# Kernel optimization log

Measured on AMD Instinct MI355X. Metric: run time of the kernel, lower is better.

The kernel has to match this reference:

```python
import jax, jax.numpy as jnp
import numpy as np

N_NODES = 50000
N_EDGES = 800000
D_IN = 128
D_OUT = 128
D_RED = 32  # out_features // reduction
ORDER = 3


def setup_inputs() -> dict:
    key = jax.random.key(0)
    ks = jax.random.split(key, 16)
    s = 1.0 / np.sqrt(D_IN)
    inp = {
        'features': jax.random.normal(ks[0], (N_NODES, D_IN), jnp.float32),
        'edge_row': jax.random.randint(ks[1], (N_EDGES,), 0, N_NODES, jnp.int32),
        'edge_col': jax.random.randint(ks[2], (N_EDGES,), 0, N_NODES, jnp.int32),
        'edge_val': jax.random.uniform(ks[3], (N_EDGES,), jnp.float32) / 16.0,  # ~1/avg_degree normalization
        'w1': jax.random.normal(ks[4], (D_IN, D_OUT), jnp.float32) * s,
        'b1': jax.random.normal(ks[5], (D_OUT,), jnp.float32) * s,
        'w2': jax.random.normal(ks[6], (D_IN, D_OUT), jnp.float32) * s,
        'b2': jax.random.normal(ks[7], (D_OUT,), jnp.float32) * s,
        'w3': jax.random.normal(ks[8], (D_IN, D_OUT), jnp.float32) * s,
        'b3': jax.random.normal(ks[9], (D_OUT,), jnp.float32) * s,
        'fc1_w': jax.random.normal(ks[10], (D_OUT, D_RED), jnp.float32) * s,
        'fc1_b': jax.random.normal(ks[11], (D_RED,), jnp.float32) * s,
        'fc2_w': jax.random.normal(ks[12], (D_RED, D_OUT), jnp.float32) * (1.0 / np.sqrt(D_RED)),
        'fc2_b': jax.random.normal(ks[13], (D_OUT,), jnp.float32) * s,
    }
    return inp


def reference(features, edge_row, edge_col, edge_val, w1, b1, w2, b2, w3, b3,
              fc1_w, fc1_b, fc2_w, fc2_b):
    def spmm(x):  # sparse [N,N] @ dense [N,D] via gather + segment_sum
        msgs = edge_val[:, None] * x[edge_col]          # [E, D]
        return jax.ops.segment_sum(msgs, edge_row, num_segments=N_NODES)

    def ngnn(w, b, order):
        h = jnp.tanh(features @ w)                      # active=True path
        for _ in range(order):                          # order spmm hops
            h = spmm(h)
        return h + b

    abstract = [ngnn(w, b, k + 1) for k, (w, b) in enumerate([(w1, b1), (w2, b2), (w3, b3)])]
    feats = jnp.stack(abstract, axis=0)                 # [order, N, D]
    m = jnp.mean(feats, axis=1)                         # [order, D]
    a = jax.nn.relu(m @ fc1_w + fc1_b) @ fc2_w + fc2_b  # [order, D]
    a = jax.nn.softmax(a, axis=0)                       # softmax over order dim
    out = jnp.einsum('ond,od->nd', feats, a)            # weighted combine
    return out
```

## Files before the change

### kernel.cpp

```cpp
#include <hip/hip_runtime.h>
#include <cstdint>

#define N_NODES 50000
#define N_EDGES 800000
#define EPCAP 64

typedef _Float16 half8 __attribute__((ext_vector_type(8)));
typedef float f32x4 __attribute__((ext_vector_type(4)));


__device__ inline unsigned pack_half2(float lo, float hi) {
    union { _Float16 h[2]; unsigned u; } cv;
    cv.h[0] = (_Float16)lo; cv.h[1] = (_Float16)hi;
    return cv.u;
}
__device__ inline float h_lo(unsigned u) {
    union { unsigned u; _Float16 h[2]; } cv; cv.u = u; return (float)cv.h[0];
}
__device__ inline float h_hi(unsigned u) {
    union { unsigned u; _Float16 h[2]; } cv; cv.u = u; return (float)cv.h[1];
}


__global__ __launch_bounds__(256) void scatter_wprep_kernel(const int* __restrict__ rows,
                                                            const int* __restrict__ cols,
                                                            const float* __restrict__ vals,
                                                            int* __restrict__ cnt,
                                                            unsigned* __restrict__ ep,
                                                            const float* __restrict__ w3,
                                                            const float* __restrict__ w2,
                                                            const float* __restrict__ w1,
                                                            _Float16* __restrict__ Wt) {
    int bx = blockIdx.x;
    if (bx >= 3125) {
        int b = bx - 3125;
        const float* W = (b == 0) ? w3 : (b == 1) ? w2 : w1;
        _Float16* O = Wt + (size_t)b * 16384;
        for (int i = threadIdx.x; i < 16384; i += 256) {
            int j = i >> 7, d = i & 127;
            O[j * 128 + d] = (_Float16)W[d * 128 + j];
        }
        return;
    }
    int e = bx * 256 + threadIdx.x;
    int r = rows[e];
    int p = atomicAdd(&cnt[r], 1);
    union { _Float16 h; unsigned short s; } cv; cv.h = (_Float16)vals[e];
    if (p < EPCAP)
        __builtin_nontemporal_store(((unsigned)cv.s << 16) | (unsigned)cols[e],
                                    &ep[(size_t)r * EPCAP + p]);
}


__global__ __launch_bounds__(256) void gemm_mfma3_kernel(const float* __restrict__ F,
                                                         const _Float16* __restrict__ Wt,
                                                         unsigned* __restrict__ T1, int nrows) {
    __shared__ _Float16 Fs[64 * 128];
    __shared__ _Float16 Ws[128 * 128];
    int tid = threadIdx.x;
    int lane = tid & 63, wv = tid >> 6;
    int c = lane & 15, g = lane >> 4;
    int rowbase = blockIdx.x * 64;

    for (int i = tid; i < 4096; i += 256) {
        int r = i >> 6;
        int row = rowbase + r; if (row >= nrows) row = nrows - 1;
        float2 fv = ((const float2*)F)[(size_t)row * 64 + (i & 63)];
        *(unsigned*)((char*)Fs + ((i * 4) ^ ((r & 15) << 4))) = pack_half2(fv.x, fv.y);
    }
    __syncthreads();

    half8 afr[4];
    #pragma unroll
    for (int ks = 0; ks < 4; ++ks) {
        int off = (((wv * 16 + c) * 128 + ks * 32 + g * 8) * 2) ^ (c << 4);
        afr[ks] = *(const half8*)((const char*)Fs + off);
    }

    for (int b = 0; b < 3; ++b) {
        const unsigned* WtU = (const unsigned*)(Wt + (size_t)b * 16384);
        for (int i = tid; i < 8192; i += 256) {
            int j = i >> 6;
            *(unsigned*)((char*)Ws + ((i * 4) ^ ((j & 15) << 4))) = WtU[i];
        }
        __syncthreads();

        f32x4 zero = {0.f, 0.f, 0.f, 0.f};
        f32x4 acc[8];
        #pragma unroll
        for (int t = 0; t < 8; ++t) acc[t] = zero;

        #pragma unroll
        for (int ks = 0; ks < 4; ++ks) {
            #pragma unroll
            for (int t = 0; t < 8; ++t) {
                int j = t * 16 + c;
                int off = ((j * 128 + ks * 32 + g * 8) * 2) ^ ((j & 15) << 4);
                half8 bfr = *(const half8*)((const char*)Ws + off);
                acc[t] = __builtin_amdgcn_mfma_f32_16x16x32_f16(afr[ks], bfr, acc[t], 0, 0, 0);
            }
        }

        #pragma unroll
        for (int t = 0; t < 4; ++t) {
            int j = t * 16 + c;
            #pragma unroll
            for (int r = 0; r < 4; ++r) {
                int row = rowbase + wv * 16 + g * 4 + r;
                if (row < N_NODES)
                    T1[(size_t)row * 192 + b * 64 + j] =
                        pack_half2(tanhf(acc[t][r]), tanhf(acc[t + 4][r]));
            }
        }
        __syncthreads();
    }
}


template <int NCHUNK>
__global__ __launch_bounds__(512) void spmm_stage_kernel(const int* __restrict__ cnts,
                                                         const unsigned* __restrict__ ep,
                                                         const unsigned* __restrict__ x,
                                                         unsigned* __restrict__ ob0,
                                                         unsigned* __restrict__ obf,
                                                         float* __restrict__ csumK) {
    __shared__ float cs[128];
    int tid = threadIdx.x;
    if (tid < 128) cs[tid] = 0.f;
    __syncthreads();

    int row = blockIdx.x * 8 + (tid >> 6);
    int lane = tid & 63;
    int n = __builtin_amdgcn_readfirstlane(cnts[row]);
    n = n < EPCAP ? n : EPCAP;
    const unsigned* e0 = ep + (size_t)row * EPCAP;

    float ax[NCHUNK], ay[NCHUNK];
    #pragma unroll
    for (int cc = 0; cc < NCHUNK; ++cc) { ax[cc] = 0.f; ay[cc] = 0.f; }

    const unsigned* xl = x + lane;
    constexpr int U = 8;
    int i = 0;
    for (; i + U <= n; i += U) {
        unsigned p[U];
        #pragma unroll
        for (int u = 0; u < U; ++u) p[u] = e0[i + u];
        unsigned gx[U][NCHUNK];
        #pragma unroll
        for (int u = 0; u < U; ++u) {
            unsigned b = (p[u] & 0xFFFFu) * (unsigned)(NCHUNK * 64);
            #pragma unroll
            for (int cc = 0; cc < NCHUNK; ++cc) gx[u][cc] = xl[b + cc * 64];
        }
        #pragma unroll
        for (int u = 0; u < U; ++u) {
            union { unsigned short s; _Float16 h; } cu; cu.s = (unsigned short)(p[u] >> 16);
            float v = (float)cu.h;
            #pragma unroll
            for (int cc = 0; cc < NCHUNK; ++cc) {
                ax[cc] += v * h_lo(gx[u][cc]);
                ay[cc] += v * h_hi(gx[u][cc]);
            }
        }
    }
    for (; i < n; ++i) {
        unsigned p = e0[i];
        unsigned b = (p & 0xFFFFu) * (unsigned)(NCHUNK * 64);
        union { unsigned short s; _Float16 h; } cu; cu.s = (unsigned short)(p >> 16);
        float v = (float)cu.h;
        #pragma unroll
        for (int cc = 0; cc < NCHUNK; ++cc) {
            unsigned gg = xl[b + cc * 64];
            ax[cc] += v * h_lo(gg);
            ay[cc] += v * h_hi(gg);
        }
    }

    #pragma unroll
    for (int cc = 0; cc < NCHUNK - 1; ++cc)
        ob0[(size_t)row * ((NCHUNK - 1) * 64) + cc * 64 + lane] = pack_half2(ax[cc], ay[cc]);

    float fx = ax[NCHUNK - 1], fy = ay[NCHUNK - 1];
    obf[(size_t)row * 64 + lane] = pack_half2(fx, fy);
    atomicAdd(&cs[2 * lane + 0], fx);
    atomicAdd(&cs[2 * lane + 1], fy);
    __syncthreads();
    if (tid < 128) atomicAdd(&csumK[(blockIdx.x & 7) * 384 + tid], cs[tid]);
}


__global__ __launch_bounds__(256) void combine_kernel(float* __restrict__ out,
                                                      const unsigned* __restrict__ f1,
                                                      const unsigned* __restrict__ f2,
                                                      const unsigned* __restrict__ f3,
                                                      const float* __restrict__ csum,
                                                      const float* __restrict__ b1,
                                                      const float* __restrict__ b2,
                                                      const float* __restrict__ b3,
                                                      const float* __restrict__ fc1w,
                                                      const float* __restrict__ fc1b,
                                                      const float* __restrict__ fc2w,
                                                      const float* __restrict__ fc2b) {
    __shared__ float m[3][128];
    __shared__ float rr[3][32];
    __shared__ float wgt[3][128];
    int t = threadIdx.x;

    if (t < 128) {
        const float inv = 1.0f / (float)N_NODES;
        int slot = (t < 64) ? (2 * t) : (2 * (t - 64) + 1);
        #pragma unroll
        for (int k = 0; k < 3; ++k) {
            float s = 0.f;
            #pragma unroll
            for (int rep = 0; rep < 8; ++rep) s += csum[rep * 384 + k * 128 + slot];
            const float* bk = (k == 0) ? b1 : (k == 1) ? b2 : b3;
            m[k][t] = s * inv + bk[t];
        }
    }
    __syncthreads();
    if (t < 96) {
        int k = t >> 5, j = t & 31;
        float acc = fc1b[j];
        for (int d = 0; d < 128; ++d) acc += m[k][d] * fc1w[d * 32 + j];
        rr[k][j] = fmaxf(acc, 0.f);
    }
    __syncthreads();
    if (t < 128) {
        float a[3];
        #pragma unroll
        for (int k = 0; k < 3; ++k) {
            float acc = fc2b[t];
            for (int j = 0; j < 32; ++j) acc += rr[k][j] * fc2w[j * 128 + t];
            a[k] = acc;
        }
        float mx = fmaxf(a[0], fmaxf(a[1], a[2]));
        float e0 = expf(a[0] - mx), e1 = expf(a[1] - mx), e2 = expf(a[2] - mx);
        float s = e0 + e1 + e2;
        wgt[0][t] = e0 / s;
        wgt[1][t] = e1 / s;
        wgt[2][t] = e2 / s;
    }
    __syncthreads();

    const int total = N_NODES * 32;
    int idx0 = blockIdx.x * blockDim.x + threadIdx.x;
    int stride = gridDim.x * blockDim.x;
    int qb = idx0 & 31;
    float4 W0 = *(const float4*)&wgt[0][qb * 4];
    float4 W1 = *(const float4*)&wgt[1][qb * 4];
    float4 W2 = *(const float4*)&wgt[2][qb * 4];
    float4 B1 = ((const float4*)b1)[qb];
    float4 B2 = ((const float4*)b2)[qb];
    float4 B3 = ((const float4*)b3)[qb];
    bool hi = qb >= 16;
    int qm = qb & 15;
    for (int idx = idx0; idx < total; idx += stride) {
        int row = idx >> 5;
        uint4 u1 = ((const uint4*)f1)[row * 16 + qm];
        uint4 u2 = ((const uint4*)f2)[row * 16 + qm];
        uint4 u3 = ((const uint4*)f3)[row * 16 + qm];
        float f1x = hi ? h_hi(u1.x) : h_lo(u1.x);
        float f1y = hi ? h_hi(u1.y) : h_lo(u1.y);
        float f1z = hi ? h_hi(u1.z) : h_lo(u1.z);
        float f1w = hi ? h_hi(u1.w) : h_lo(u1.w);
        float f2x = hi ? h_hi(u2.x) : h_lo(u2.x);
        float f2y = hi ? h_hi(u2.y) : h_lo(u2.y);
        float f2z = hi ? h_hi(u2.z) : h_lo(u2.z);
        float f2w = hi ? h_hi(u2.w) : h_lo(u2.w);
        float f3x = hi ? h_hi(u3.x) : h_lo(u3.x);
        float f3y = hi ? h_hi(u3.y) : h_lo(u3.y);
        float f3z = hi ? h_hi(u3.z) : h_lo(u3.z);
        float f3w = hi ? h_hi(u3.w) : h_lo(u3.w);
        float4 o;
        o.x = (f1x + B1.x) * W0.x + (f2x + B2.x) * W1.x + (f3x + B3.x) * W2.x;
        o.y = (f1y + B1.y) * W0.y + (f2y + B2.y) * W1.y + (f3y + B3.y) * W2.y;
        o.z = (f1z + B1.z) * W0.z + (f2z + B2.z) * W1.z + (f3z + B3.z) * W2.z;
        o.w = (f1w + B1.w) * W0.w + (f2w + B2.w) * W1.w + (f3w + B3.w) * W2.w;
        ((float4*)out)[idx] = o;
    }
}


extern "C" void kernel_launch(void* const* d_in, const int* in_sizes, int n_in,
                              void* d_out, int out_size, void* d_ws, size_t ws_size,
                              hipStream_t stream) {
    const float* F    = (const float*)d_in[0];
    const int*   erow = (const int*)d_in[1];
    const int*   ecol = (const int*)d_in[2];
    const float* eval_ = (const float*)d_in[3];
    const float* w1 = (const float*)d_in[4];  const float* b1 = (const float*)d_in[5];
    const float* w2 = (const float*)d_in[6];  const float* b2 = (const float*)d_in[7];
    const float* w3 = (const float*)d_in[8];  const float* b3 = (const float*)d_in[9];
    const float* fc1w = (const float*)d_in[10]; const float* fc1b = (const float*)d_in[11];
    const float* fc2w = (const float*)d_in[12]; const float* fc2b = (const float*)d_in[13];
    float* out = (float*)d_out;

    char* ws = (char*)d_ws;
    size_t off = 0;
    auto alloc = [&](size_t bytes) -> void* {
        off = (off + 255) & ~(size_t)255;
        void* p = ws + off;
        off += bytes;
        return p;
    };
    unsigned* T1   = (unsigned*)alloc((size_t)N_NODES * 192 * 4);
    unsigned* T2   = (unsigned*)alloc((size_t)N_NODES * 128 * 4);
    unsigned* T3   = (unsigned*)alloc((size_t)N_NODES * 64 * 4);
    unsigned* f1h  = (unsigned*)alloc((size_t)N_NODES * 64 * 4);
    unsigned* ep   = (unsigned*)alloc((size_t)N_NODES * EPCAP * 4);
    int*   counts  = (int*)alloc((size_t)N_NODES * sizeof(int));
    float* csum    = (float*)alloc(8 * 3 * 128 * sizeof(float));
    _Float16* Wt   = (_Float16*)alloc(3 * 16384 * sizeof(_Float16));
    unsigned* f2h  = T1;
    unsigned* f3h  = T1 + (size_t)N_NODES * 64;

    size_t zlen = (size_t)((char*)csum + 8 * 3 * 128 * sizeof(float) - (char*)counts);
    hipMemsetAsync(counts, 0, zlen, stream);

    scatter_wprep_kernel<<<3125 + 3, 256, 0, stream>>>(erow, ecol, eval_, counts, ep,
                                                       w3, w2, w1, Wt);
    gemm_mfma3_kernel<<<(N_NODES + 63) / 64, 256, 0, stream>>>(F, Wt, T1, N_NODES);

    const int spmmGrid = N_NODES / 8;

    spmm_stage_kernel<3><<<spmmGrid, 512, 0, stream>>>(counts, ep, T1, T2, f1h, csum + 0 * 128);
    spmm_stage_kernel<2><<<spmmGrid, 512, 0, stream>>>(counts, ep, T2, T3, f2h, csum + 1 * 128);
    spmm_stage_kernel<1><<<spmmGrid, 512, 0, stream>>>(counts, ep, T3, nullptr, f3h, csum + 2 * 128);

    combine_kernel<<<2048, 256, 0, stream>>>(out, f1h, f2h, f3h, csum, b1, b2, b3,
                                             fc1w, fc1b, fc2w, fc2b);
}
```

Measured before the change: 352.1 us.

## Fuse final SpMM hop with combine using column-sum trick for third-order mean

```diff
diff --git a/kernel.cpp b/kernel.cpp
--- a/kernel.cpp
+++ b/kernel.cpp
@@ -27,6 +27,7 @@
                                                             const float* __restrict__ vals,
                                                             int* __restrict__ cnt,
                                                             unsigned* __restrict__ ep,
+                                                            float* __restrict__ qsum,
                                                             const float* __restrict__ w3,
                                                             const float* __restrict__ w2,
                                                             const float* __restrict__ w1,
@@ -44,11 +45,13 @@
     }
     int e = bx * 256 + threadIdx.x;
     int r = rows[e];
+    int c = cols[e];
     int p = atomicAdd(&cnt[r], 1);
     union { _Float16 h; unsigned short s; } cv; cv.h = (_Float16)vals[e];
     if (p < EPCAP)
-        __builtin_nontemporal_store(((unsigned)cv.s << 16) | (unsigned)cols[e],
+        __builtin_nontemporal_store(((unsigned)cv.s << 16) | (unsigned)c,
                                     &ep[(size_t)r * EPCAP + p]);
+    atomicAdd(&qsum[c], (float)cv.h);
 }
 
 
@@ -117,13 +120,12 @@
 }
 
 
-template <int NCHUNK>
-__global__ __launch_bounds__(512) void spmm_stage_kernel(const int* __restrict__ cnts,
-                                                         const unsigned* __restrict__ ep,
-                                                         const unsigned* __restrict__ x,
-                                                         unsigned* __restrict__ ob0,
-                                                         unsigned* __restrict__ obf,
-                                                         float* __restrict__ csumK) {
+__global__ __launch_bounds__(512) void spmm1_kernel(const int* __restrict__ cnts,
+                                                    const unsigned* __restrict__ ep,
+                                                    const unsigned* __restrict__ x,
+                                                    unsigned* __restrict__ ob0,
+                                                    unsigned* __restrict__ obf,
+                                                    float* __restrict__ csum) {
     __shared__ float cs[128];
     int tid = threadIdx.x;
     if (tid < 128) cs[tid] = 0.f;
@@ -135,10 +137,7 @@
     n = n < EPCAP ? n : EPCAP;
     const unsigned* e0 = ep + (size_t)row * EPCAP;
 
-    float ax[NCHUNK], ay[NCHUNK];
-    #pragma unroll
-    for (int cc = 0; cc < NCHUNK; ++cc) { ax[cc] = 0.f; ay[cc] = 0.f; }
-
+    float ax[3] = {0.f, 0.f, 0.f}, ay[3] = {0.f, 0.f, 0.f};
     const unsigned* xl = x + lane;
     constexpr int U = 8;
     int i = 0;
@@ -146,19 +145,19 @@
         unsigned p[U];
         #pragma unroll
         for (int u = 0; u < U; ++u) p[u] = e0[i + u];
-        unsigned gx[U][NCHUNK];
+        unsigned gx[U][3];
         #pragma unroll
         for (int u = 0; u < U; ++u) {
-            unsigned b = (p[u] & 0xFFFFu) * (unsigned)(NCHUNK * 64);
+            unsigned b = (p[u] & 0xFFFFu) * 192u;
             #pragma unroll
-            for (int cc = 0; cc < NCHUNK; ++cc) gx[u][cc] = xl[b + cc * 64];
+            for (int cc = 0; cc < 3; ++cc) gx[u][cc] = xl[b + cc * 64];
         }
         #pragma unroll
         for (int u = 0; u < U; ++u) {
             union { unsigned short s; _Float16 h; } cu; cu.s = (unsigned short)(p[u] >> 16);
             float v = (float)cu.h;
             #pragma unroll
-            for (int cc = 0; cc < NCHUNK; ++cc) {
+            for (int cc = 0; cc < 3; ++cc) {
                 ax[cc] += v * h_lo(gx[u][cc]);
                 ay[cc] += v * h_hi(gx[u][cc]);
             }
@@ -166,120 +165,194 @@
     }
     for (; i < n; ++i) {
         unsigned p = e0[i];
-        unsigned b = (p & 0xFFFFu) * (unsigned)(NCHUNK * 64);
+        unsigned b = (p & 0xFFFFu) * 192u;
         union { unsigned short s; _Float16 h; } cu; cu.s = (unsigned short)(p >> 16);
         float v = (float)cu.h;
         #pragma unroll
-        for (int cc = 0; cc < NCHUNK; ++cc) {
+        for (int cc = 0; cc < 3; ++cc) {
             unsigned gg = xl[b + cc * 64];
             ax[cc] += v * h_lo(gg);
             ay[cc] += v * h_hi(gg);
         }
     }
 
-    #pragma unroll
-    for (int cc = 0; cc < NCHUNK - 1; ++cc)
-        ob0[(size_t)row * ((NCHUNK - 1) * 64) + cc * 64 + lane] = pack_half2(ax[cc], ay[cc]);
-
-    float fx = ax[NCHUNK - 1], fy = ay[NCHUNK - 1];
-    obf[(size_t)row * 64 + lane] = pack_half2(fx, fy);
-    atomicAdd(&cs[2 * lane + 0], fx);
-    atomicAdd(&cs[2 * lane + 1], fy);
-    __syncthreads();
-    if (tid < 128) atomicAdd(&csumK[(blockIdx.x & 7) * 384 + tid], cs[tid]);
-}
-
-
-__global__ __launch_bounds__(256) void combine_kernel(float* __restrict__ out,
-                                                      const unsigned* __restrict__ f1,
-                                                      const unsigned* __restrict__ f2,
-                                                      const unsigned* __restrict__ f3,
-                                                      const float* __restrict__ csum,
-                                                      const float* __restrict__ b1,
-                                                      const float* __restrict__ b2,
-                                                      const float* __restrict__ b3,
-                                                      const float* __restrict__ fc1w,
-                                                      const float* __restrict__ fc1b,
-                                                      const float* __restrict__ fc2w,
-                                                      const float* __restrict__ fc2b) {
+    ob0[(size_t)row * 128 + 0 * 64 + lane] = pack_half2(ax[0], ay[0]);
+    ob0[(size_t)row * 128 + 1 * 64 + lane] = pack_half2(ax[1], ay[1]);
+    obf[(size_t)row * 64 + lane] = pack_half2(ax[2], ay[2]);
+    atomicAdd(&cs[2 * lane + 0], ax[2]);
+    atomicAdd(&cs[2 * lane + 1], ay[2]);
+    __syncthreads();
+    if (tid < 128) atomicAdd(&csum[(blockIdx.x & 7) * 384 + tid], cs[tid]);
+}
+
+
+__global__ __launch_bounds__(512) void spmm2_kernel(const int* __restrict__ cnts,
+                                                    const unsigned* __restrict__ ep,
+                                                    const unsigned* __restrict__ x,
+                                                    unsigned* __restrict__ T3,
+                                                    unsigned* __restrict__ f2h,
+                                                    const float* __restrict__ qsum,
+                                                    float* __restrict__ csum) {
+    __shared__ float cs[256];
+    int tid = threadIdx.x;
+    if (tid < 256) cs[tid] = 0.f;
+    __syncthreads();
+
+    int row = blockIdx.x * 8 + (tid >> 6);
+    int lane = tid & 63;
+    int n = __builtin_amdgcn_readfirstlane(cnts[row]);
+    n = n < EPCAP ? n : EPCAP;
+    const unsigned* e0 = ep + (size_t)row * EPCAP;
+
+    float ax0 = 0.f, ay0 = 0.f, ax1 = 0.f, ay1 = 0.f;
+    const unsigned* xl = x + lane;
+    constexpr int U = 8;
+    int i = 0;
+    for (; i + U <= n; i += U) {
+        unsigned p[U];
+        #pragma unroll
+        for (int u = 0; u < U; ++u) p[u] = e0[i + u];
+        unsigned g0[U], g1[U];
+        #pragma unroll
+        for (int u = 0; u < U; ++u) {
+            unsigned b = (p[u] & 0xFFFFu) * 128u;
+            g0[u] = xl[b];
+            g1[u] = xl[b + 64];
+        }
+        #pragma unroll
+        for (int u = 0; u < U; ++u) {
+            union { unsigned short s; _Float16 h; } cu; cu.s = (unsigned short)(p[u] >> 16);
+            float v = (float)cu.h;
+            ax0 += v * h_lo(g0[u]); ay0 += v * h_hi(g0[u]);
+            ax1 += v * h_lo(g1[u]); ay1 += v * h_hi(g1[u]);
+        }
+    }
+    for (; i < n; ++i) {
+        unsigned p = e0[i];
+        unsigned b = (p & 0xFFFFu) * 128u;
+        union { unsigned short s; _Float16 h; } cu; cu.s = (unsigned short)(p >> 16);
+        float v = (float)cu.h;
+        unsigned g0 = xl[b], g1 = xl[b + 64];
+        ax0 += v * h_lo(g0); ay0 += v * h_hi(g0);
+        ax1 += v * h_lo(g1); ay1 += v * h_hi(g1);
+    }
+
+    T3[(size_t)row * 64 + lane] = pack_half2(ax0, ay0);
+    float qr = qsum[row];
+    atomicAdd(&cs[128 + 2 * lane + 0], qr * ax0);
+    atomicAdd(&cs[128 + 2 * lane + 1], qr * ay0);
+    f2h[(size_t)row * 64 + lane] = pack_half2(ax1, ay1);
+    atomicAdd(&cs[2 * lane + 0], ax1);
+    atomicAdd(&cs[2 * lane + 1], ay1);
+    __syncthreads();
+    if (tid < 256) atomicAdd(&csum[(blockIdx.x & 7) * 384 + 128 + tid], cs[tid]);
+}
+
+
+__global__ __launch_bounds__(512) void spmm3_combine_kernel(const int* __restrict__ cnts,
+                                                            const unsigned* __restrict__ ep,
+                                                            const unsigned* __restrict__ x,
+                                                            const unsigned* __restrict__ f1h,
+                                                            const unsigned* __restrict__ f2h,
+                                                            const float* __restrict__ csum,
+                                                            const float* __restrict__ b1,
+                                                            const float* __restrict__ b2,
+                                                            const float* __restrict__ b3,
+                                                            const float* __restrict__ fc1w,
+                                                            const float* __restrict__ fc1b,
+                                                            const float* __restrict__ fc2w,
+                                                            const float* __restrict__ fc2b,
+                                                            float* __restrict__ out) {
     __shared__ float m[3][128];
     __shared__ float rr[3][32];
-    __shared__ float wgt[3][128];
-    int t = threadIdx.x;
-
-    if (t < 128) {
+    __shared__ float wgtS[3][128];
+    int tid = threadIdx.x;
+
+    if (tid < 128) {
         const float inv = 1.0f / (float)N_NODES;
-        int slot = (t < 64) ? (2 * t) : (2 * (t - 64) + 1);
+        int slot = (tid < 64) ? (2 * tid) : (2 * (tid - 64) + 1);
         #pragma unroll
         for (int k = 0; k < 3; ++k) {
             float s = 0.f;
             #pragma unroll
             for (int rep = 0; rep < 8; ++rep) s += csum[rep * 384 + k * 128 + slot];
             const float* bk = (k == 0) ? b1 : (k == 1) ? b2 : b3;
-            m[k][t] = s * inv + bk[t];
-        }
-    }
-    __syncthreads();
-    if (t < 96) {
-        int k = t >> 5, j = t & 31;
+            m[k][tid] = s * inv + bk[tid];
+        }
+    }
+    __syncthreads();
+    if (tid < 96) {
+        int k = tid >> 5, j = tid & 31;
         float acc = fc1b[j];
         for (int d = 0; d < 128; ++d) acc += m[k][d] * fc1w[d * 32 + j];
         rr[k][j] = fmaxf(acc, 0.f);
     }
     __syncthreads();
-    if (t < 128) {
+    if (tid < 128) {
         float a[3];
         #pragma unroll
         for (int k = 0; k < 3; ++k) {
-            float acc = fc2b[t];
-            for (int j = 0; j < 32; ++j) acc += rr[k][j] * fc2w[j * 128 + t];
+            float acc = fc2b[tid];
+            for (int j = 0; j < 32; ++j) acc += rr[k][j] * fc2w[j * 128 + tid];
             a[k] = acc;
         }
         float mx = fmaxf(a[0], fmaxf(a[1], a[2]));
         float e0 = expf(a[0] - mx), e1 = expf(a[1] - mx), e2 = expf(a[2] - mx);
         float s = e0 + e1 + e2;
-        wgt[0][t] = e0 / s;
-        wgt[1][t] = e1 / s;
-        wgt[2][t] = e2 / s;
-    }
-    __syncthreads();
-
-    const int total = N_NODES * 32;
-    int idx0 = blockIdx.x * blockDim.x + threadIdx.x;
-    int stride = gridDim.x * blockDim.x;
-    int qb = idx0 & 31;
-    float4 W0 = *(const float4*)&wgt[0][qb * 4];
-    float4 W1 = *(const float4*)&wgt[1][qb * 4];
-    float4 W2 = *(const float4*)&wgt[2][qb * 4];
-    float4 B1 = ((const float4*)b1)[qb];
-    float4 B2 = ((const float4*)b2)[qb];
-    float4 B3 = ((const float4*)b3)[qb];
-    bool hi = qb >= 16;
-    int qm = qb & 15;
-    for (int idx = idx0; idx < total; idx += stride) {
-        int row = idx >> 5;
-        uint4 u1 = ((const uint4*)f1)[row * 16 + qm];
-        uint4 u2 = ((const uint4*)f2)[row * 16 + qm];
-        uint4 u3 = ((const uint4*)f3)[row * 16 + qm];
-        float f1x = hi ? h_hi(u1.x) : h_lo(u1.x);
-        float f1y = hi ? h_hi(u1.y) : h_lo(u1.y);
-        float f1z = hi ? h_hi(u1.z) : h_lo(u1.z);
-        float f1w = hi ? h_hi(u1.w) : h_lo(u1.w);
-        float f2x = hi ? h_hi(u2.x) : h_lo(u2.x);
-        float f2y = hi ? h_hi(u2.y) : h_lo(u2.y);
-        float f2z = hi ? h_hi(u2.z) : h_lo(u2.z);
-        float f2w = hi ? h_hi(u2.w) : h_lo(u2.w);
-        float f3x = hi ? h_hi(u3.x) : h_lo(u3.x);
-        float f3y = hi ? h_hi(u3.y) : h_lo(u3.y);
-        float f3z = hi ? h_hi(u3.z) : h_lo(u3.z);
-        float f3w = hi ? h_hi(u3.w) : h_lo(u3.w);
-        float4 o;
-        o.x = (f1x + B1.x) * W0.x + (f2x + B2.x) * W1.x + (f3x + B3.x) * W2.x;
-        o.y = (f1y + B1.y) * W0.y + (f2y + B2.y) * W1.y + (f3y + B3.y) * W2.y;
-        o.z = (f1z + B1.z) * W0.z + (f2z + B2.z) * W1.z + (f3z + B3.z) * W2.z;
-        o.w = (f1w + B1.w) * W0.w + (f2w + B2.w) * W1.w + (f3w + B3.w) * W2.w;
-        ((float4*)out)[idx] = o;
-    }
+        wgtS[0][tid] = e0 / s;
+        wgtS[1][tid] = e1 / s;
+        wgtS[2][tid] = e2 / s;
+    }
+    __syncthreads();
+
+    int lane = tid & 63;
+    int row = blockIdx.x * 8 + (tid >> 6);
+
+    float g0lo = wgtS[0][lane], g0hi = wgtS[0][lane + 64];
+    float g1lo = wgtS[1][lane], g1hi = wgtS[1][lane + 64];
+    float g2lo = wgtS[2][lane], g2hi = wgtS[2][lane + 64];
+    float b1lo = b1[lane], b1hi = b1[lane + 64];
+    float b2lo = b2[lane], b2hi = b2[lane + 64];
+    float b3lo = b3[lane], b3hi = b3[lane + 64];
+
+    int n = __builtin_amdgcn_readfirstlane(cnts[row]);
+    n = n < EPCAP ? n : EPCAP;
+    const unsigned* e0 = ep + (size_t)row * EPCAP;
+    const unsigned* xl = x + lane;
+
+    float fx = 0.f, fy = 0.f;
+    constexpr int U = 8;
+    int i = 0;
+    for (; i + U <= n; i += U) {
+        unsigned p[U];
+        #pragma unroll
+        for (int u = 0; u < U; ++u) p[u] = e0[i + u];
+        unsigned gg[U];
+        #pragma unroll
+        for (int u = 0; u < U; ++u) gg[u] = xl[(p[u] & 0xFFFFu) * 64u];
+        #pragma unroll
+        for (int u = 0; u < U; ++u) {
+            union { unsigned short s; _Float16 h; } cu; cu.s = (unsigned short)(p[u] >> 16);
+            float v = (float)cu.h;
+            fx += v * h_lo(gg[u]);
+            fy += v * h_hi(gg[u]);
+        }
+    }
+    for (; i < n; ++i) {
+        unsigned p = e0[i];
+        unsigned gg = xl[(p & 0xFFFFu) * 64u];
+        union { unsigned short s; _Float16 h; } cu; cu.s = (unsigned short)(p >> 16);
+        float v = (float)cu.h;
+        fx += v * h_lo(gg);
+        fy += v * h_hi(gg);
+    }
+
+    unsigned u1 = f1h[(size_t)row * 64 + lane];
+    unsigned u2 = f2h[(size_t)row * 64 + lane];
+    out[(size_t)row * 128 + lane] =
+        (h_lo(u1) + b1lo) * g0lo + (h_lo(u2) + b2lo) * g1lo + (fx + b3lo) * g2lo;
+    out[(size_t)row * 128 + 64 + lane] =
+        (h_hi(u1) + b1hi) * g0hi + (h_hi(u2) + b2hi) * g1hi + (fy + b3hi) * g2hi;
 }
 
 
@@ -312,23 +385,23 @@
     unsigned* ep   = (unsigned*)alloc((size_t)N_NODES * EPCAP * 4);
     int*   counts  = (int*)alloc((size_t)N_NODES * sizeof(int));
     float* csum    = (float*)alloc(8 * 3 * 128 * sizeof(float));
+    float* qsum    = (float*)alloc((size_t)N_NODES * sizeof(float));
     _Float16* Wt   = (_Float16*)alloc(3 * 16384 * sizeof(_Float16));
     unsigned* f2h  = T1;
-    unsigned* f3h  = T1 + (size_t)N_NODES * 64;
-
-    size_t zlen = (size_t)((char*)csum + 8 * 3 * 128 * sizeof(float) - (char*)counts);
+    unsigned* f3s  = T1 + (size_t)N_NODES * 64;
+    (void)f3s;
+
+    size_t zlen = (size_t)((char*)qsum + (size_t)N_NODES * sizeof(float) - (char*)counts);
     hipMemsetAsync(counts, 0, zlen, stream);
 
-    scatter_wprep_kernel<<<3125 + 3, 256, 0, stream>>>(erow, ecol, eval_, counts, ep,
+    scatter_wprep_kernel<<<3125 + 3, 256, 0, stream>>>(erow, ecol, eval_, counts, ep, qsum,
                                                        w3, w2, w1, Wt);
     gemm_mfma3_kernel<<<(N_NODES + 63) / 64, 256, 0, stream>>>(F, Wt, T1, N_NODES);
 
     const int spmmGrid = N_NODES / 8;
 
-    spmm_stage_kernel<3><<<spmmGrid, 512, 0, stream>>>(counts, ep, T1, T2, f1h, csum + 0 * 128);
-    spmm_stage_kernel<2><<<spmmGrid, 512, 0, stream>>>(counts, ep, T2, T3, f2h, csum + 1 * 128);
-    spmm_stage_kernel<1><<<spmmGrid, 512, 0, stream>>>(counts, ep, T3, nullptr, f3h, csum + 2 * 128);
-
-    combine_kernel<<<2048, 256, 0, stream>>>(out, f1h, f2h, f3h, csum, b1, b2, b3,
-                                             fc1w, fc1b, fc2w, fc2b);
-}
+    spmm1_kernel<<<spmmGrid, 512, 0, stream>>>(counts, ep, T1, T2, f1h, csum);
+    spmm2_kernel<<<spmmGrid, 512, 0, stream>>>(counts, ep, T2, T3, f2h, qsum, csum);
+    spmm3_combine_kernel<<<spmmGrid, 512, 0, stream>>>(counts, ep, T3, f1h, f2h, csum,
+                                                       b1, b2, b3, fc1w, fc1b, fc2w, fc2b, out);
+}
```

Result: slower. 409.1 us (+16.2%).
